# Optimization experiments

Hardware: AMD Instinct MI355X
Metric: run time of the kernel (lower is better)

## Reference

```python
import jax, jax.numpy as jnp
import numpy as np

B, S, D, F, E = 2, 1024, 1024, 4096, 8

def setup_inputs() -> dict:
    key = jax.random.key(0)
    ks = jax.random.split(key, 4)
    s = 0.02
    return {
        "x": jax.random.normal(ks[0], (B, S, D), dtype=jnp.float32),
        "switch_w": jax.random.normal(ks[1], (D, E), dtype=jnp.float32) * s,
        "switch_b": jnp.zeros((E,), dtype=jnp.float32),
        "w1": jax.random.normal(ks[2], (E, D, F), dtype=jnp.float32) * s,
        "b1": jnp.zeros((E, F), dtype=jnp.float32),
        "w2": jax.random.normal(ks[3], (E, F, D), dtype=jnp.float32) * s,
        "b2": jnp.zeros((E, D), dtype=jnp.float32),
    }

def reference(x, switch_w, switch_b, w1, b1, w2, b2):
    b, s, d = x.shape
    xt = x.reshape(-1, d)                               # [T, D]
    logits = xt @ switch_w + switch_b                   # [T, E]
    route_prob = jax.nn.softmax(logits, axis=-1)        # [T, E]
    route_prob_max = jnp.max(route_prob, axis=-1)       # [T]
    routes = jnp.argmax(route_prob, axis=-1)            # [T] int
    onehot = jax.nn.one_hot(routes, E, dtype=xt.dtype)  # [T, E]
    counts = onehot.sum(axis=0)                         # tokens per expert (float, as in torch new_tensor)

    # top-1 dispatch: run each expert FFN, keep only its tokens via mask (drop_tokens=False -> no capacity drop)
    def body(acc, params):
        W1, B1, W2, B2, mask = params                   # mask: [T]
        y = jax.nn.relu(xt @ W1 + B1) @ W2 + B2         # [T, D]
        return acc + mask[:, None] * y, None

    out, _ = jax.lax.scan(body, jnp.zeros_like(xt), (w1, b1, w2, b2, onehot.T))
    out = out * route_prob_max[:, None]                 # is_scale_prob=True
    final_output = out.reshape(b, s, d)
    return final_output, counts, route_prob.sum(axis=0), 0, route_prob_max
```

## Files before the change

kernel.cpp:

```cpp
#include <hip/hip_runtime.h>
#include <stdint.h>

#define T_TOK 2048
#define D_DIM 1024
#define F_DIM 4096
#define E_NUM 8
#define RPMAX 4096
#define BK 64

typedef __attribute__((ext_vector_type(8))) short bfx8;
typedef __attribute__((ext_vector_type(4))) float fx4;

__device__ __forceinline__ unsigned short f2bf(float f) {
  union { float f; uint32_t u; } v; v.f = f;
  uint32_t u = v.u;
  u += 0x7FFFu + ((u >> 16) & 1u);
  return (unsigned short)(u >> 16);
}

__device__ __forceinline__ void load_lds16(const unsigned short* g, unsigned short* l) {
  __builtin_amdgcn_global_load_lds(
      (const __attribute__((address_space(1))) void*)g,
      (__attribute__((address_space(3))) void*)l, 16, 0, 0);
}

__device__ __forceinline__ uint32_t cvtpk_bf16(float lo, float hi) {
  uint32_t d;
  asm("v_cvt_pk_bf16_f32 %0, %1, %2" : "=v"(d) : "v"(lo), "v"(hi));
  return d;
}

__global__ __launch_bounds__(256) void router_kernel(
    const float* __restrict__ x, const float* __restrict__ sw,
    const float* __restrict__ sb, float* __restrict__ pmax_out,
    int* __restrict__ routes, float* __restrict__ probs,
    unsigned short* __restrict__ xbf) {
  const int wave = threadIdx.x >> 6, lane = threadIdx.x & 63;
  const int t = blockIdx.x * 4 + wave;
  const float* xr = x + (size_t)t * D_DIM;
  float acc[8];
#pragma unroll
  for (int e = 0; e < 8; ++e) acc[e] = 0.f;
#pragma unroll
  for (int i = 0; i < 4; ++i) {
    const int d = i * 256 + lane * 4;
    float4 xv = *(const float4*)(xr + d);
    ushort4 h;
    h.x = f2bf(xv.x); h.y = f2bf(xv.y); h.z = f2bf(xv.z); h.w = f2bf(xv.w);
    *(ushort4*)(xbf + (size_t)t * D_DIM + d) = h;
    const float xs[4] = {xv.x, xv.y, xv.z, xv.w};
#pragma unroll
    for (int j = 0; j < 4; ++j) {
      const float4* swp = (const float4*)(sw + (size_t)(d + j) * 8);
      float4 w0 = swp[0], w1 = swp[1];
      acc[0] += xs[j] * w0.x; acc[1] += xs[j] * w0.y;
      acc[2] += xs[j] * w0.z; acc[3] += xs[j] * w0.w;
      acc[4] += xs[j] * w1.x; acc[5] += xs[j] * w1.y;
      acc[6] += xs[j] * w1.z; acc[7] += xs[j] * w1.w;
    }
  }
#pragma unroll
  for (int e = 0; e < 8; ++e) {
    float v = acc[e];
    for (int o = 32; o > 0; o >>= 1) v += __shfl_down(v, o, 64);
    acc[e] = v;
  }
  if (lane == 0) {
#pragma unroll
    for (int e = 0; e < 8; ++e) acc[e] += sb[e];
    int am = 0; float mx = acc[0];
#pragma unroll
    for (int e = 1; e < 8; ++e) if (acc[e] > mx) { mx = acc[e]; am = e; }
    float p[8]; float s = 0.f;
#pragma unroll
    for (int e = 0; e < 8; ++e) { p[e] = expf(acc[e] - mx); s += p[e]; }
    float inv = 1.0f / s;
    pmax_out[t] = inv;
    routes[t] = am;
#pragma unroll
    for (int e = 0; e < 8; ++e) probs[(size_t)t * 8 + e] = p[e] * inv;
  }
}

__global__ __launch_bounds__(256) void plan_kernel(
    const int* __restrict__ routes, const float* __restrict__ probs,
    int* __restrict__ off, int* __restrict__ perm_out, int* __restrict__ perm_src,
    float* __restrict__ out_counts, float* __restrict__ out_psums,
    float* __restrict__ out_zero) {
  __shared__ int cnt[8];
  __shared__ int cur[8];
  __shared__ int offs[9];
  __shared__ float red[256][8];
  const int tid = threadIdx.x;
  if (tid < 8) cnt[tid] = 0;
  for (int i = tid; i < RPMAX; i += 256) { perm_out[i] = -1; perm_src[i] = 0; }
  __syncthreads();
  float loc[8];
#pragma unroll
  for (int e = 0; e < 8; ++e) loc[e] = 0.f;
  for (int t = tid; t < T_TOK; t += 256) {
    atomicAdd(&cnt[routes[t]], 1);
    const float4* p = (const float4*)(probs + (size_t)t * 8);
    float4 a = p[0], b = p[1];
    loc[0] += a.x; loc[1] += a.y; loc[2] += a.z; loc[3] += a.w;
    loc[4] += b.x; loc[5] += b.y; loc[6] += b.z; loc[7] += b.w;
  }
#pragma unroll
  for (int e = 0; e < 8; ++e) red[tid][e] = loc[e];
  __syncthreads();
  for (int s = 128; s >= 1; s >>= 1) {
    if (tid < s) {
#pragma unroll
      for (int e = 0; e < 8; ++e) red[tid][e] += red[tid + s][e];
    }
    __syncthreads();
  }
  if (tid == 0) {
    int o = 0;
    for (int e = 0; e < 8; ++e) { offs[e] = o; o += ((cnt[e] + 255) >> 8) << 8; }
    offs[8] = o;
    *out_zero = 0.0f;
  }
  __syncthreads();
  if (tid < 9) off[tid] = offs[tid];
  if (tid < 8) {
    cur[tid] = offs[tid];
    out_counts[tid] = (float)cnt[tid];
    out_psums[tid] = red[0][tid];
  }
  __syncthreads();
  for (int t = tid; t < T_TOK; t += 256) {
    int e = routes[t];
    int pos = atomicAdd(&cur[e], 1);
    perm_out[pos] = t;
    perm_src[pos] = t;
  }
}

__global__ __launch_bounds__(256) void gather_kernel(
    const unsigned short* __restrict__ xbf, const int* __restrict__ off,
    const int* __restrict__ perm_src, unsigned short* __restrict__ xg) {
  const int wave = threadIdx.x >> 6, lane = threadIdx.x & 63;
  const int row = blockIdx.x * 4 + wave;
  if (row >= off[8]) return;
  const int tok = perm_src[row];
  const bfx8* s = (const bfx8*)(xbf + (size_t)tok * D_DIM);
  bfx8* d = (bfx8*)(xg + (size_t)row * D_DIM);
  d[lane] = s[lane];
  d[lane + 64] = s[lane + 64];
}

__global__ __launch_bounds__(256) void reduce_kernel(
    const float* __restrict__ P, const int* __restrict__ off,
    const int* __restrict__ perm_out, const float* __restrict__ b2,
    const float* __restrict__ pmax, float* __restrict__ out) {
  const int row = blockIdx.x;
  if (row >= off[8]) return;
  const int tok = perm_out[row];
  if (tok < 0) return;
  int e = 0;
#pragma unroll
  for (int i = 1; i <= 7; ++i) if (row >= off[i]) e = i;
  const int col = threadIdx.x * 4;
  const size_t base = (size_t)row * D_DIM + col;
  float4 p0 = *(const float4*)(P + base);
  float4 p1 = *(const float4*)(P + (size_t)1 * RPMAX * D_DIM + base);
  float4 p2 = *(const float4*)(P + (size_t)2 * RPMAX * D_DIM + base);
  float4 p3 = *(const float4*)(P + (size_t)3 * RPMAX * D_DIM + base);
  float4 bv = *(const float4*)(b2 + (size_t)e * D_DIM + col);
  const float pm = pmax[tok];
  float4 r;
  r.x = (p0.x + p1.x + p2.x + p3.x + bv.x) * pm;
  r.y = (p0.y + p1.y + p2.y + p3.y + bv.y) * pm;
  r.z = (p0.z + p1.z + p2.z + p3.z + bv.z) * pm;
  r.w = (p0.w + p1.w + p2.w + p3.w + bv.w) * pm;
  *(float4*)(out + (size_t)tok * D_DIM + col) = r;
}

template <int K_, int N_>
__global__ __launch_bounds__(512, 4) void gemm1s(
    const unsigned short* __restrict__ A,
    const float* __restrict__ W,
    const float* __restrict__ Bias,
    const int* __restrict__ off,
    unsigned short* __restrict__ Hout) {
  constexpr int BM = 128, BN = 128;
  constexpr int NT = K_ / BK;
  constexpr int FM = 4, FN = 2;
  constexpr int NBX = N_ / BN;
  __shared__ __align__(16) unsigned short As[BM * 64];
  __shared__ __align__(16) unsigned short Bs[BN * 64];
  const int tid = threadIdx.x;
  const int bid = blockIdx.x;
  const int live_by = off[8] >> 7;
  const int live = live_by * NBX;
  if (bid >= live) return;
  const int chunk = live >> 3;
  const int newlin = (bid & 7) * chunk + (bid >> 3);
  const int bx = newlin / live_by;
  const int by = newlin % live_by;
  const int rowbase = by * BM;
  int e = 0;
#pragma unroll
  for (int i = 1; i <= 7; ++i) if (rowbase >= off[i]) e = i;
  const int n0 = bx * BN;
  const int wave = tid >> 6, lane = tid & 63;
  const int wm = wave >> 2, wn = wave & 3;
  const float* Wn0 = W + (size_t)e * K_ * N_ + n0;

  const unsigned short* aSrc[2];
#pragma unroll
  for (int c = 0; c < 2; ++c) {
    int ca = (wave * 2 + c) * 64 + lane;
    int row = ca >> 3, slot = ca & 7;
    int sc = slot ^ (row & 7);
    aSrc[c] = A + (size_t)(rowbase + row) * K_ + sc * 8;
  }

  const int nq = lane & 15;
  const int qg = lane >> 4;
  const int kq = (qg & 1) * 4;
  const int cb = qg >> 1;
  fx4 br[4];

  fx4 acc[FM][FN];
#pragma unroll
  for (int a = 0; a < FM; ++a)
#pragma unroll
    for (int b = 0; b < FN; ++b) acc[a][b] = (fx4){0.f, 0.f, 0.f, 0.f};

  for (int t = 0; t < NT; ++t) {
    const int kt = t * BK;
#pragma unroll
    for (int c = 0; c < 2; ++c)
      load_lds16(aSrc[c] + kt, As + (wave * 2 + c) * 512);
#pragma unroll
    for (int j = 0; j < 4; ++j)
      br[j] = *(const fx4*)(Wn0 + (size_t)(kt + wave * 8 + kq + j) * N_ +
                            cb * 64 + nq * 4);
#pragma unroll
    for (int i = 0; i < 4; ++i) {
      const int nl = cb * 64 + nq * 4 + i;
      const int key = ((nl >> 2) + 2 * (nl & 3)) & 7;
      uint32_t d0 = cvtpk_bf16(br[0][i], br[1][i]);
      uint32_t d1 = cvtpk_bf16(br[2][i], br[3][i]);
      *(uint2*)(Bs + nl * 64 + (wave ^ key) * 8 + kq) = make_uint2(d0, d1);
    }
    __syncthreads();
#pragma unroll
    for (int kk = 0; kk < 2; ++kk) {
      bfx8 af[FM], bf[FN];
#pragma unroll
      for (int fm = 0; fm < FM; ++fm) {
        int r = wm * 64 + fm * 16 + (lane & 15);
        int c = (kk * 4 + (lane >> 4)) ^ (r & 7);
        af[fm] = *(const bfx8*)(As + r * 64 + c * 8);
      }
#pragma unroll
      for (int fn = 0; fn < FN; ++fn) {
        int nn = wn * 32 + fn * 16 + (lane & 15);
        int key = ((nn >> 2) + 2 * (nn & 3)) & 7;
        int c = (kk * 4 + (lane >> 4)) ^ key;
        bf[fn] = *(const bfx8*)(Bs + nn * 64 + c * 8);
      }
#pragma unroll
      for (int fm = 0; fm < FM; ++fm)
#pragma unroll
        for (int fn = 0; fn < FN; ++fn)
          acc[fm][fn] = __builtin_amdgcn_mfma_f32_16x16x32_bf16(
              af[fm], bf[fn], acc[fm][fn], 0, 0, 0);
    }
    __syncthreads();
  }

  const int colbase = n0 + wn * 32;
#pragma unroll
  for (int fn = 0; fn < FN; ++fn) {
    int colg = colbase + fn * 16 + (lane & 15);
    float bv = Bias[(size_t)e * N_ + colg];
#pragma unroll
    for (int fm = 0; fm < FM; ++fm) {
      int rg = rowbase + wm * 64 + fm * 16 + ((lane >> 4) << 2);
#pragma unroll
      for (int j = 0; j < 4; ++j) {
        float v = fmaxf(acc[fm][fn][j] + bv, 0.f);
        Hout[(size_t)(rg + j) * N_ + colg] = f2bf(v);
      }
    }
  }
}

template <int K_, int N_, int KSPLIT>
__global__ __launch_bounds__(512, 4) void gemm2s(
    const unsigned short* __restrict__ A,
    const float* __restrict__ W,
    const int* __restrict__ off,
    float* __restrict__ Pout) {
  constexpr int BM = 128, BN = 256;
  constexpr int KS = K_ / KSPLIT;
  constexpr int NT = KS / BK;
  constexpr int FM = 4, FN = 4, GRP = 2;
  constexpr int NBX = N_ / BN;
  __shared__ __align__(16) unsigned short As[BM * 64];
  __shared__ __align__(16) unsigned short Bs[BN * 64];
  const int tid = threadIdx.x;
  const int bid = blockIdx.x;
  const int live_by = off[8] >> 7;
  const int live = live_by * NBX * KSPLIT;
  if (bid >= live) return;
  const int chunk = live >> 3;
  const int newlin = (bid & 7) * chunk + (bid >> 3);
  const int bx = newlin / (live_by * KSPLIT);
  const int rem = newlin % (live_by * KSPLIT);
  const int by = rem % live_by;
  const int kz = rem / live_by;
  const int rowbase = by * BM;
  int e = 0;
#pragma unroll
  for (int i = 1; i <= 7; ++i) if (rowbase >= off[i]) e = i;
  const int n0 = bx * BN;
  const int k0base = kz * KS;
  const int wave = tid >> 6, lane = tid & 63;
  const int wm = wave >> 2, wn = wave & 3;
  const float* Wn0 = W + (size_t)e * K_ * N_ + n0;

  const unsigned short* aSrc[2];
#pragma unroll
  for (int c = 0; c < 2; ++c) {
    int ca = (wave * 2 + c) * 64 + lane;
    int row = ca >> 3, slot = ca & 7;
    int sc = slot ^ (row & 7);
    aSrc[c] = A + (size_t)(rowbase + row) * K_ + k0base + sc * 8;
  }

  const int nq = lane & 15;
  const int qg = lane >> 4;
  const int kq = (qg & 1) * 4;
  fx4 br[GRP][4];

  fx4 acc[FM][FN];
#pragma unroll
  for (int a = 0; a < FM; ++a)
#pragma unroll
    for (int b = 0; b < FN; ++b) acc[a][b] = (fx4){0.f, 0.f, 0.f, 0.f};

  for (int t = 0; t < NT; ++t) {
    const int kt = t * BK;
#pragma unroll
    for (int c = 0; c < 2; ++c)
      load_lds16(aSrc[c] + kt, As + (wave * 2 + c) * 512);
#pragma unroll
    for (int g = 0; g < GRP; ++g) {
      const int cb = g * 2 + (qg >> 1);
#pragma unroll
      for (int j = 0; j < 4; ++j)
        br[g][j] = *(const fx4*)(Wn0 + (size_t)(kt + wave * 8 + kq + j) * N_ +
                                 cb * 64 + nq * 4);
    }
#pragma unroll
    for (int g = 0; g < GRP; ++g) {
      const int cb = g * 2 + (qg >> 1);
#pragma unroll
      for (int i = 0; i < 4; ++i) {
        const int nl = cb * 64 + nq * 4 + i;
        const int key = ((nl >> 2) + 2 * (nl & 3)) & 7;
        uint32_t d0 = cvtpk_bf16(br[g][0][i], br[g][1][i]);
        uint32_t d1 = cvtpk_bf16(br[g][2][i], br[g][3][i]);
        *(uint2*)(Bs + nl * 64 + (wave ^ key) * 8 + kq) = make_uint2(d0, d1);
      }
    }
    __syncthreads();
#pragma unroll
    for (int kk = 0; kk < 2; ++kk) {
      bfx8 af[FM], bf[FN];
#pragma unroll
      for (int fm = 0; fm < FM; ++fm) {
        int r = wm * 64 + fm * 16 + (lane & 15);
        int c = (kk * 4 + (lane >> 4)) ^ (r & 7);
        af[fm] = *(const bfx8*)(As + r * 64 + c * 8);
      }
#pragma unroll
      for (int fn = 0; fn < FN; ++fn) {
        int nn = wn * 64 + fn * 16 + (lane & 15);
        int key = ((nn >> 2) + 2 * (nn & 3)) & 7;
        int c = (kk * 4 + (lane >> 4)) ^ key;
        bf[fn] = *(const bfx8*)(Bs + nn * 64 + c * 8);
      }
#pragma unroll
      for (int fm = 0; fm < FM; ++fm)
#pragma unroll
        for (int fn = 0; fn < FN; ++fn)
          acc[fm][fn] = __builtin_amdgcn_mfma_f32_16x16x32_bf16(
              af[fm], bf[fn], acc[fm][fn], 0, 0, 0);
    }
    __syncthreads();
  }

  const int colbase = n0 + wn * 64;
  float* Pk = Pout + (size_t)kz * RPMAX * N_;
#pragma unroll
  for (int fm = 0; fm < FM; ++fm) {
    int rg = rowbase + wm * 64 + fm * 16 + ((lane >> 4) << 2);
#pragma unroll
    for (int j = 0; j < 4; ++j) {
#pragma unroll
      for (int fn = 0; fn < FN; ++fn) {
        int colg = colbase + fn * 16 + (lane & 15);
        Pk[(size_t)(rg + j) * N_ + colg] = acc[fm][fn][j];
      }
    }
  }
}

extern "C" void kernel_launch(void* const* d_in, const int* in_sizes, int n_in,
                              void* d_out, int out_size, void* d_ws, size_t ws_size,
                              hipStream_t stream) {
  const float* x  = (const float*)d_in[0];
  const float* sw = (const float*)d_in[1];
  const float* sb = (const float*)d_in[2];
  const float* w1 = (const float*)d_in[3];
  const float* b1 = (const float*)d_in[4];
  const float* w2 = (const float*)d_in[5];
  const float* b2 = (const float*)d_in[6];
  float* out = (float*)d_out;

  char* ws = (char*)d_ws;
  int*   off      = (int*)(ws + 0);
  int*   routes   = (int*)(ws + 1024);
  int*   perm_out = (int*)(ws + 16384);
  int*   perm_src = (int*)(ws + 32768);
  float* probs    = (float*)(ws + 65536);
  unsigned short* xbf = (unsigned short*)(ws + (1u << 20));
  unsigned short* H   = (unsigned short*)(ws + (8u << 20));
  unsigned short* xg  = (unsigned short*)(ws + (40u << 20));
  float* P            = (float*)(ws + (48u << 20));

  float* out_final  = out;
  float* out_counts = out + 2097152;
  float* out_psums  = out + 2097160;
  float* out_zero   = out + 2097168;
  float* out_pmax   = out + 2097169;

  router_kernel<<<T_TOK / 4, 256, 0, stream>>>(x, sw, sb, out_pmax, routes, probs, xbf);
  plan_kernel<<<1, 256, 0, stream>>>(routes, probs, off, perm_out, perm_src,
                                     out_counts, out_psums, out_zero);
  gather_kernel<<<RPMAX / 4, 256, 0, stream>>>(xbf, off, perm_src, xg);

  gemm1s<D_DIM, F_DIM><<<1024, 512, 0, stream>>>(xg, w1, b1, off, H);
  gemm2s<F_DIM, D_DIM, 4><<<512, 512, 0, stream>>>(H, w2, off, P);
  reduce_kernel<<<RPMAX, 256, 0, stream>>>(P, off, perm_out, b2, out_pmax, out_final);
}
```

Baseline: 150.0 us.

## Pre-convert expert W1 to padded bf16 before first expert GEMM

```diff
diff --git a/kernel.cpp b/kernel.cpp
--- a/kernel.cpp
+++ b/kernel.cpp
@@ -7,6 +7,8 @@
 #define E_NUM 8
 #define RPMAX 4096
 #define BK 64
+#define PITCH_W 4224
+#define PITCH_X 1088
 
 typedef __attribute__((ext_vector_type(8))) short bfx8;
 typedef __attribute__((ext_vector_type(4))) float fx4;
@@ -145,9 +147,24 @@
   if (row >= off[8]) return;
   const int tok = perm_src[row];
   const bfx8* s = (const bfx8*)(xbf + (size_t)tok * D_DIM);
-  bfx8* d = (bfx8*)(xg + (size_t)row * D_DIM);
+  bfx8* d = (bfx8*)(xg + (size_t)row * PITCH_X);
   d[lane] = s[lane];
   d[lane + 64] = s[lane + 64];
+}
+
+__global__ __launch_bounds__(256) void convb_kernel(
+    const float* __restrict__ W, unsigned short* __restrict__ Wbf) {
+  const size_t row = blockIdx.x;
+  const float* src = W + row * F_DIM;
+  unsigned short* dst = Wbf + row * PITCH_W;
+  const int t = threadIdx.x;
+#pragma unroll
+  for (int s = 0; s < 4; ++s) {
+    float4 v = *(const float4*)(src + s * 1024 + t * 4);
+    ushort4 h;
+    h.x = f2bf(v.x); h.y = f2bf(v.y); h.z = f2bf(v.z); h.w = f2bf(v.w);
+    *(ushort4*)(dst + s * 1024 + t * 4) = h;
+  }
 }
 
 __global__ __launch_bounds__(256) void reduce_kernel(
@@ -180,7 +197,7 @@
 template <int K_, int N_>
 __global__ __launch_bounds__(512, 4) void gemm1s(
     const unsigned short* __restrict__ A,
-    const float* __restrict__ W,
+    const unsigned short* __restrict__ Wbf,
     const float* __restrict__ Bias,
     const int* __restrict__ off,
     unsigned short* __restrict__ Hout) {
@@ -206,7 +223,7 @@
   const int n0 = bx * BN;
   const int wave = tid >> 6, lane = tid & 63;
   const int wm = wave >> 2, wn = wave & 3;
-  const float* Wn0 = W + (size_t)e * K_ * N_ + n0;
+  const unsigned short* Wn0 = Wbf + (size_t)e * K_ * PITCH_W + n0;
 
   const unsigned short* aSrc[2];
 #pragma unroll
@@ -214,14 +231,14 @@
     int ca = (wave * 2 + c) * 64 + lane;
     int row = ca >> 3, slot = ca & 7;
     int sc = slot ^ (row & 7);
-    aSrc[c] = A + (size_t)(rowbase + row) * K_ + sc * 8;
+    aSrc[c] = A + (size_t)(rowbase + row) * PITCH_X + sc * 8;
   }
 
   const int nq = lane & 15;
   const int qg = lane >> 4;
   const int kq = (qg & 1) * 4;
   const int cb = qg >> 1;
-  fx4 br[4];
+  ushort4 bu[4];
 
   fx4 acc[FM][FN];
 #pragma unroll
@@ -236,14 +253,18 @@
       load_lds16(aSrc[c] + kt, As + (wave * 2 + c) * 512);
 #pragma unroll
     for (int j = 0; j < 4; ++j)
-      br[j] = *(const fx4*)(Wn0 + (size_t)(kt + wave * 8 + kq + j) * N_ +
-                            cb * 64 + nq * 4);
+      bu[j] = *(const ushort4*)(Wn0 + (size_t)(kt + wave * 8 + kq + j) * PITCH_W +
+                                cb * 64 + nq * 4);
 #pragma unroll
     for (int i = 0; i < 4; ++i) {
       const int nl = cb * 64 + nq * 4 + i;
       const int key = ((nl >> 2) + 2 * (nl & 3)) & 7;
-      uint32_t d0 = cvtpk_bf16(br[0][i], br[1][i]);
-      uint32_t d1 = cvtpk_bf16(br[2][i], br[3][i]);
+      const unsigned short* p0 = (const unsigned short*)&bu[0];
+      const unsigned short* p1 = (const unsigned short*)&bu[1];
+      const unsigned short* p2 = (const unsigned short*)&bu[2];
+      const unsigned short* p3 = (const unsigned short*)&bu[3];
+      uint32_t d0 = (uint32_t)p0[i] | ((uint32_t)p1[i] << 16);
+      uint32_t d1 = (uint32_t)p2[i] | ((uint32_t)p3[i] << 16);
       *(uint2*)(Bs + nl * 64 + (wave ^ key) * 8 + kq) = make_uint2(d0, d1);
     }
     __syncthreads();
@@ -433,7 +454,8 @@
   unsigned short* xbf = (unsigned short*)(ws + (1u << 20));
   unsigned short* H   = (unsigned short*)(ws + (8u << 20));
   unsigned short* xg  = (unsigned short*)(ws + (40u << 20));
-  float* P            = (float*)(ws + (48u << 20));
+  unsigned short* Wbf = (unsigned short*)(ws + (49u << 20));
+  float* P            = (float*)(ws + (49u << 20));
 
   float* out_final  = out;
   float* out_counts = out + 2097152;
@@ -446,7 +468,9 @@
                                      out_counts, out_psums, out_zero);
   gather_kernel<<<RPMAX / 4, 256, 0, stream>>>(xbf, off, perm_src, xg);
 
-  gemm1s<D_DIM, F_DIM><<<1024, 512, 0, stream>>>(xg, w1, b1, off, H);
+  convb_kernel<<<E_NUM * D_DIM, 256, 0, stream>>>(w1, Wbf);
+
+  gemm1s<D_DIM, F_DIM><<<1024, 512, 0, stream>>>(xg, Wbf, b1, off, H);
   gemm2s<F_DIM, D_DIM, 4><<<512, 512, 0, stream>>>(H, w2, off, P);
   reduce_kernel<<<RPMAX, 256, 0, stream>>>(P, off, perm_out, b2, out_pmax, out_final);
 }
```

Result: slower. 156.3 us (+4.2%).
